# Optimization experiments

Measured on AMD Instinct MI355X. Metric: run time of the kernel, lower is better.

The kernel has to match this reference:

```python
import jax, jax.numpy as jnp
import numpy as np

BN_EPS = 1e-5
NN_EPS = 1e-8
K = 3


def conv_bn_relu(x, W, b, gamma, beta, mean, var):
    # x: [B, Cin, N]; W: [Cout, Cin] (1x1 conv); BN in inference mode w/ running stats
    y = jnp.einsum('bcn,oc->bon', x, W) + b[None, :, None]
    y = (y - mean[None, :, None]) * (gamma / jnp.sqrt(var + BN_EPS))[None, :, None] + beta[None, :, None]
    return jax.nn.relu(y)


def three_interpolation(p1, p2, f2):
    # p1: [B, N1, 3] unknown xyz; p2: [B, N2, 3] known xyz; f2: [B, C, N2]
    # squared pairwise distances via the expansion trick (avoids [B,N1,N2,3])
    d2 = (jnp.sum(p1 * p1, -1)[:, :, None]
          + jnp.sum(p2 * p2, -1)[:, None, :]
          - 2.0 * jnp.einsum('bnd,bmd->bnm', p1, p2))  # [B, N1, N2]
    neg_d2, idx = jax.lax.top_k(-d2, K)                 # 3 nearest
    dist = -neg_d2                                      # squared dists, [B, N1, 3]
    recip = 1.0 / (dist + NN_EPS)
    weight = recip / jnp.sum(recip, axis=-1, keepdims=True)  # [B, N1, 3]
    f2t = jnp.transpose(f2, (0, 2, 1))                  # [B, N2, C]
    gathered = jax.vmap(lambda f, i: f[i])(f2t, idx)    # [B, N1, 3, C]
    return jnp.einsum('bnkc,bnk->bcn', gathered, weight)  # [B, C, N1]


def setup_inputs() -> dict:
    key = jax.random.key(0)
    ks = jax.random.split(key, 16)
    B, N1, N2 = 8, 16384, 4096
    mlp = [256, 128, 128]
    inp = {
        'p1': jax.random.normal(ks[0], (B, N1, 3), jnp.float32),
        'p2': jax.random.normal(ks[1], (B, N2, 3), jnp.float32),
        'f2': jax.random.normal(ks[2], (B, mlp[0], N2), jnp.float32),
    }
    kidx = 3
    for li in range(len(mlp) - 1):
        cin, cout = mlp[li], mlp[li + 1]
        inp[f'W{li}'] = jax.random.normal(ks[kidx], (cout, cin), jnp.float32) * (1.0 / np.sqrt(cin)); kidx += 1
        inp[f'b{li}'] = jnp.zeros((cout,), jnp.float32)
        inp[f'gamma{li}'] = jnp.ones((cout,), jnp.float32)
        inp[f'beta{li}'] = jnp.zeros((cout,), jnp.float32)
        inp[f'mean{li}'] = jax.random.normal(ks[kidx], (cout,), jnp.float32) * 0.1; kidx += 1
        inp[f'var{li}'] = jax.random.uniform(ks[kidx], (cout,), jnp.float32, 0.5, 1.5); kidx += 1
    return inp


def reference(p1, p2, f2,
              W0, b0, gamma0, beta0, mean0, var0,
              W1, b1, gamma1, beta1, mean1, var1):
    f = conv_bn_relu(f2, W0, b0, gamma0, beta0, mean0, var0)
    f = conv_bn_relu(f, W1, b1, gamma1, beta1, mean1, var1)
    return three_interpolation(p1, p2, f)
```

## Files before the change

kernel.cpp:

```cpp
#include <hip/hip_runtime.h>

#define B_    8
#define N1_   16384
#define N2_   4096
#define NTOT_ (B_ * N1_)

__device__ __forceinline__ float np_sumsq(float x, float y, float z)
{
#pragma clang fp contract(off)
    return ((x * x + y * y) + z * z);
}

__global__ __launch_bounds__(256) void fold_kernel(
    const float* __restrict__ W, const float* __restrict__ bias,
    const float* __restrict__ gamma, const float* __restrict__ beta,
    const float* __restrict__ mean, const float* __restrict__ var,
    float* __restrict__ Wp, float* __restrict__ bp, int Cout, int Cin)
{
    int t = blockIdx.x * 256 + threadIdx.x;
    if (t < Cout * Cin) {
        int o = t / Cin;
        float s = gamma[o] / sqrtf(var[o] + 1e-5f);
        Wp[t] = W[t] * s;
    }
    if (t < Cout) {
        float s = gamma[t] / sqrtf(var[t] + 1e-5f);
        bp[t] = beta[t] + (bias[t] - mean[t]) * s;
    }
}

__global__ __launch_bounds__(256) void q4_kernel(
    const float* __restrict__ p2, float4* __restrict__ q4)
{
    int t = blockIdx.x * 256 + threadIdx.x;
    float x = p2[3 * (size_t)t + 0];
    float y = p2[3 * (size_t)t + 1];
    float z = p2[3 * (size_t)t + 2];
    q4[t] = make_float4(x, y, z, np_sumsq(x, y, z));
}

template <int CIN, bool TRANS>
__global__ __launch_bounds__(256) void gemm_relu_kernel(
    const float* __restrict__ X, const float* __restrict__ Wp,
    const float* __restrict__ bp, float* __restrict__ Y)
{
    __shared__ float A_lds[32][136];
    __shared__ float B_lds[32][128];

    const int b  = blockIdx.y;
    const int n0 = blockIdx.x * 128;
    const int tid = threadIdx.x;
    const int ty = tid >> 4;
    const int tx = tid & 15;
    const float* Xb = X + (size_t)b * CIN * N2_;

    float acc[8][8];
#pragma unroll
    for (int i = 0; i < 8; ++i)
#pragma unroll
        for (int j = 0; j < 8; ++j) acc[i][j] = 0.f;

    const int a_kq = (tid & 7) * 4;
    const int a_r0 = tid >> 3;
    const int b_n4 = (tid & 31) * 4;
    const int b_k0 = tid >> 5;

    for (int k0 = 0; k0 < CIN; k0 += 32) {
#pragma unroll
        for (int i = 0; i < 4; ++i) {
            const int row = a_r0 + 32 * i;
            const float4 v = *(const float4*)&Wp[(size_t)row * CIN + k0 + a_kq];
            A_lds[a_kq + 0][row] = v.x;
            A_lds[a_kq + 1][row] = v.y;
            A_lds[a_kq + 2][row] = v.z;
            A_lds[a_kq + 3][row] = v.w;
        }
#pragma unroll
        for (int i = 0; i < 4; ++i) {
            const int krow = b_k0 + 8 * i;
            *(float4*)&B_lds[krow][b_n4] =
                *(const float4*)&Xb[(size_t)(k0 + krow) * N2_ + n0 + b_n4];
        }
        __syncthreads();

#pragma unroll
        for (int kk = 0; kk < 32; ++kk) {
            const float4 a0 = *(const float4*)&A_lds[kk][ty * 4];
            const float4 a1 = *(const float4*)&A_lds[kk][64 + ty * 4];
            const float4 bq0 = *(const float4*)&B_lds[kk][tx * 4];
            const float4 bq1 = *(const float4*)&B_lds[kk][64 + tx * 4];
            const float av[8] = {a0.x, a0.y, a0.z, a0.w, a1.x, a1.y, a1.z, a1.w};
            const float bv[8] = {bq0.x, bq0.y, bq0.z, bq0.w, bq1.x, bq1.y, bq1.z, bq1.w};
#pragma unroll
            for (int i = 0; i < 8; ++i)
#pragma unroll
                for (int j = 0; j < 8; ++j)
                    acc[i][j] = fmaf(av[i], bv[j], acc[i][j]);
        }
        __syncthreads();
    }

    float bias_v[8];
#pragma unroll
    for (int i = 0; i < 8; ++i) {
        const int r = (i < 4) ? (ty * 4 + i) : (64 + ty * 4 + (i - 4));
        bias_v[i] = bp[r];
    }

    if (!TRANS) {
#pragma unroll
        for (int i = 0; i < 8; ++i) {
            const int r = (i < 4) ? (ty * 4 + i) : (64 + ty * 4 + (i - 4));
            float* yrow = Y + ((size_t)b * 128 + r) * N2_ + n0;
            float4 v0, v1;
            v0.x = fmaxf(acc[i][0] + bias_v[i], 0.f);
            v0.y = fmaxf(acc[i][1] + bias_v[i], 0.f);
            v0.z = fmaxf(acc[i][2] + bias_v[i], 0.f);
            v0.w = fmaxf(acc[i][3] + bias_v[i], 0.f);
            v1.x = fmaxf(acc[i][4] + bias_v[i], 0.f);
            v1.y = fmaxf(acc[i][5] + bias_v[i], 0.f);
            v1.z = fmaxf(acc[i][6] + bias_v[i], 0.f);
            v1.w = fmaxf(acc[i][7] + bias_v[i], 0.f);
            *(float4*)(yrow + tx * 4) = v0;
            *(float4*)(yrow + 64 + tx * 4) = v1;
        }
    } else {
        float (*T)[132] = (float(*)[132])&A_lds[0][0];
#pragma unroll
        for (int s = 0; s < 4; ++s) {
            if ((tx >> 3) == (s & 1)) {
                const int joff = (s >> 1) * 4;
                const int cl0 = (tx & 7) * 4;
#pragma unroll
                for (int i = 0; i < 8; ++i) {
                    const int r = (i < 4) ? (ty * 4 + i) : (64 + ty * 4 + (i - 4));
#pragma unroll
                    for (int j = 0; j < 4; ++j)
                        T[cl0 + j][r] = fmaxf(acc[i][j + joff] + bias_v[i], 0.f);
                }
            }
            __syncthreads();
#pragma unroll
            for (int p = 0; p < 4; ++p) {
                const int row = (tid >> 5) + 8 * p;
                const float4 v = *(const float4*)&T[row][(tid & 31) * 4];
                float* orow = Y + ((size_t)b * N2_ + n0 + 32 * s + row) * 128;
                *(float4*)&orow[(tid & 31) * 4] = v;
            }
            __syncthreads();
        }
    }
}

__global__ __launch_bounds__(256, 8) void knn_phase1(
    const float* __restrict__ p1, const float4* __restrict__ q4,
    float* __restrict__ part_d, int* __restrict__ part_i)
{
    __shared__ float4 qs[1024];
    const int tid = threadIdx.x;
    const int chunk = blockIdx.x & 3;
    const int g = (blockIdx.x >> 2) * 256 + tid;
    const int b = g >> 14;

    const float px = p1[3 * (size_t)g + 0];
    const float py = p1[3 * (size_t)g + 1];
    const float pz = p1[3 * (size_t)g + 2];
    const float s1 = np_sumsq(px, py, pz);

    const float4* qb = q4 + (size_t)b * N2_ + chunk * 1024;
#pragma unroll
    for (int i = 0; i < 4; ++i) qs[tid + i * 256] = qb[tid + i * 256];
    __syncthreads();

    float d0 = 1e30f, d1 = 1e30f, d2v = 1e30f;
    int i0 = 0, i1 = 0, i2 = 0;
    const int jbase = chunk * 1024;

    for (int j = 0; j < 1024; j += 4) {
#pragma unroll
        for (int u = 0; u < 4; ++u) {
            const float4 q = qs[j + u];
            const float dot = __fmaf_rn(px, q.x, __fmaf_rn(py, q.y, __fmul_rn(pz, q.z)));
            const float ss  = s1 + q.w;
            const float t   = __fmaf_rn(-2.0f, dot, ss);
            if (t < d2v) {
                const int jj = jbase + j + u;
                const bool c1 = t < d1, c0 = t < d0;
                d2v = c1 ? d1 : t;                 i2 = c1 ? i1 : jj;
                const float nd1 = c1 ? (c0 ? d0 : t) : d1;
                const int   ni1 = c1 ? (c0 ? i0 : jj) : i1;
                d1 = nd1;                          i1 = ni1;
                d0 = c0 ? t : d0;                  i0 = c0 ? jj : i0;
            }
        }
    }

    part_d[(0 * 4 + chunk) * NTOT_ + g] = d0;
    part_d[(1 * 4 + chunk) * NTOT_ + g] = d1;
    part_d[(2 * 4 + chunk) * NTOT_ + g] = d2v;
    part_i[(0 * 4 + chunk) * NTOT_ + g] = i0;
    part_i[(1 * 4 + chunk) * NTOT_ + g] = i1;
    part_i[(2 * 4 + chunk) * NTOT_ + g] = i2;
}

__global__ __launch_bounds__(256) void knn_merge(
    const float* __restrict__ part_d, const int* __restrict__ part_i,
    int* __restrict__ idx_ws, float* __restrict__ w_ws)
{
    const int g = blockIdx.x * 256 + threadIdx.x;

    float d0 = 1e30f, d1 = 1e30f, d2v = 1e30f;
    int i0 = 0, i1 = 0, i2 = 0;

#pragma unroll
    for (int c = 0; c < 4; ++c) {
#pragma unroll
        for (int k = 0; k < 3; ++k) {
            const float t = part_d[(k * 4 + c) * NTOT_ + g];
            const int  jj = part_i[(k * 4 + c) * NTOT_ + g];
            if (t < d2v) {
                const bool c1 = t < d1, c0 = t < d0;
                d2v = c1 ? d1 : t;                 i2 = c1 ? i1 : jj;
                const float nd1 = c1 ? (c0 ? d0 : t) : d1;
                const int   ni1 = c1 ? (c0 ? i0 : jj) : i1;
                d1 = nd1;                          i1 = ni1;
                d0 = c0 ? t : d0;                  i0 = c0 ? jj : i0;
            }
        }
    }

    float w0, w1, w2;
    {
#pragma clang fp contract(off)
        const float r0 = 1.0f / (d0 + 1e-8f);
        const float r1 = 1.0f / (d1 + 1e-8f);
        const float r2 = 1.0f / (d2v + 1e-8f);
        const float rs = (r0 + r1) + r2;
        w0 = r0 / rs;
        w1 = r1 / rs;
        w2 = r2 / rs;
    }

    idx_ws[g]             = i0;
    idx_ws[NTOT_ + g]     = i1;
    idx_ws[2 * NTOT_ + g] = i2;
    w_ws[g]               = w0;
    w_ws[NTOT_ + g]       = w1;
    w_ws[2 * NTOT_ + g]   = w2;
}

__global__ __launch_bounds__(256) void gather_kernel(
    const float* __restrict__ f_t, const int* __restrict__ idx_ws,
    const float* __restrict__ w_ws, float* __restrict__ out)
{
    const int tid = threadIdx.x;
    const int lane = tid & 63, cg = tid >> 6;
    const int g = blockIdx.x * 64 + lane;
    const int b = g >> 14, n = g & 16383;

    const int i0 = idx_ws[g];
    const int i1 = idx_ws[NTOT_ + g];
    const int i2 = idx_ws[2 * NTOT_ + g];
    const float w0 = w_ws[g];
    const float w1 = w_ws[NTOT_ + g];
    const float w2 = w_ws[2 * NTOT_ + g];

    const float* base = f_t + (size_t)b * N2_ * 128 + cg * 32;
    const float4* r0 = (const float4*)(base + (size_t)i0 * 128);
    const float4* r1 = (const float4*)(base + (size_t)i1 * 128);
    const float4* r2 = (const float4*)(base + (size_t)i2 * 128);

    float acc[32];
#pragma unroll
    for (int q = 0; q < 8; ++q) {
        const float4 a = r0[q], bb = r1[q], c = r2[q];
        acc[4 * q + 0] = fmaf(w0, a.x, fmaf(w1, bb.x, w2 * c.x));
        acc[4 * q + 1] = fmaf(w0, a.y, fmaf(w1, bb.y, w2 * c.y));
        acc[4 * q + 2] = fmaf(w0, a.z, fmaf(w1, bb.z, w2 * c.z));
        acc[4 * q + 3] = fmaf(w0, a.w, fmaf(w1, bb.w, w2 * c.w));
    }

    float* ob = out + ((size_t)b * 128 + cg * 32) * N1_ + n;
#pragma unroll
    for (int c = 0; c < 32; ++c)
        __builtin_nontemporal_store(acc[c], ob + (size_t)c * N1_);
}

extern "C" void kernel_launch(void* const* d_in, const int* in_sizes, int n_in,
                              void* d_out, int out_size, void* d_ws, size_t ws_size,
                              hipStream_t stream)
{
    const float* p1  = (const float*)d_in[0];
    const float* p2  = (const float*)d_in[1];
    const float* f2  = (const float*)d_in[2];
    const float* W0  = (const float*)d_in[3];
    const float* b0  = (const float*)d_in[4];
    const float* g0  = (const float*)d_in[5];
    const float* be0 = (const float*)d_in[6];
    const float* m0  = (const float*)d_in[7];
    const float* v0  = (const float*)d_in[8];
    const float* W1  = (const float*)d_in[9];
    const float* b1  = (const float*)d_in[10];
    const float* g1  = (const float*)d_in[11];
    const float* be1 = (const float*)d_in[12];
    const float* m1  = (const float*)d_in[13];
    const float* v1  = (const float*)d_in[14];

    char* ws = (char*)d_ws;
    float4* q4  = (float4*)(ws);
    float*  W0p = (float*)(ws + (512 << 10));
    float*  b0p = (float*)(ws + (640 << 10));
    float*  W1p = (float*)(ws + (644 << 10));
    float*  b1p = (float*)(ws + (708 << 10));
    float*  h   = (float*)(ws + ((size_t)1 << 20));
    float*  f_t = (float*)(ws + ((size_t)17 << 20));
    int*    idxw= (int*)  (ws + ((size_t)33 << 20));
    float*  wgt = (float*)(ws + ((size_t)35 << 20));
    float*  pd  = (float*)(ws + ((size_t)1 << 20));
    int*    pi  = (int*)  (ws + ((size_t)9 << 20));

    fold_kernel<<<128, 256, 0, stream>>>(W0, b0, g0, be0, m0, v0, W0p, b0p, 128, 256);
    fold_kernel<<<64, 256, 0, stream>>>(W1, b1, g1, be1, m1, v1, W1p, b1p, 128, 128);
    q4_kernel<<<(B_ * N2_) / 256, 256, 0, stream>>>(p2, q4);

    gemm_relu_kernel<256, false><<<dim3(32, 8), 256, 0, stream>>>(f2, W0p, b0p, h);
    gemm_relu_kernel<128, true ><<<dim3(32, 8), 256, 0, stream>>>(h, W1p, b1p, f_t);

    knn_phase1<<<(NTOT_ / 256) * 4, 256, 0, stream>>>(p1, q4, pd, pi);
    knn_merge<<<NTOT_ / 256, 256, 0, stream>>>(pd, pi, idxw, wgt);
    gather_kernel<<<NTOT_ / 64, 256, 0, stream>>>(f_t, idxw, wgt, (float*)d_out);
}
```

Baseline: 354.5 us.

## Fuse KNN split-merge into one kernel with packed-FP32 distance pairs

Replaces the 4-way chunked KNN pass and its separate merge kernel with a single kernel. Each thread now scans all 4096 reference points, streamed into LDS in four chunks. Reference points are repacked in pairs (x0,x1,y0,y1,z0,z1,w0,w1) so that distances are computed with 2-wide vector FMAs, which can map to packed FP32 ops. The top-3 insertion is skipped when no lane in the wavefront has a candidate. This removes the partial-result round trip to global memory and one launch. In exchange there are 4x fewer blocks, so each thread does a longer serial loop, and the launch-bounds occupancy hint is dropped.

```diff
diff --git a/kernel.cpp b/kernel.cpp
--- a/kernel.cpp
+++ b/kernel.cpp
@@ -4,6 +4,8 @@
 #define N1_   16384
 #define N2_   4096
 #define NTOT_ (B_ * N1_)
+
+typedef float v2f __attribute__((ext_vector_type(2)));
 
 __device__ __forceinline__ float np_sumsq(float x, float y, float z)
 {
@@ -29,14 +31,16 @@
     }
 }
 
-__global__ __launch_bounds__(256) void q4_kernel(
-    const float* __restrict__ p2, float4* __restrict__ q4)
-{
-    int t = blockIdx.x * 256 + threadIdx.x;
-    float x = p2[3 * (size_t)t + 0];
-    float y = p2[3 * (size_t)t + 1];
-    float z = p2[3 * (size_t)t + 2];
-    q4[t] = make_float4(x, y, z, np_sumsq(x, y, z));
+__global__ __launch_bounds__(256) void q4pair_kernel(
+    const float* __restrict__ p2, float4* __restrict__ q4p)
+{
+    const int t = blockIdx.x * 256 + threadIdx.x;
+    const float* a = p2 + 6 * (size_t)t;
+    const float x0 = a[0], y0 = a[1], z0 = a[2];
+    const float x1 = a[3], y1 = a[4], z1 = a[5];
+    q4p[2 * (size_t)t + 0] = make_float4(x0, x1, y0, y1);
+    q4p[2 * (size_t)t + 1] = make_float4(z0, z1, np_sumsq(x0, y0, z0),
+                                                 np_sumsq(x1, y1, z1));
 }
 
 template <int CIN, bool TRANS>
@@ -152,14 +156,28 @@
     }
 }
 
-__global__ __launch_bounds__(256, 8) void knn_phase1(
-    const float* __restrict__ p1, const float4* __restrict__ q4,
-    float* __restrict__ part_d, int* __restrict__ part_i)
-{
-    __shared__ float4 qs[1024];
+__device__ __forceinline__ void ins3(const float t, const int jj,
+    float& d0, float& d1, float& d2v, int& i0, int& i1, int& i2)
+{
+    if (t < d2v) {
+        const bool c1 = t < d1, c0 = t < d0;
+        d2v = c1 ? d1 : t;                 i2 = c1 ? i1 : jj;
+        const float nd1 = c1 ? (c0 ? d0 : t) : d1;
+        const int   ni1 = c1 ? (c0 ? i0 : jj) : i1;
+        d1 = nd1;                          i1 = ni1;
+        d0 = c0 ? t : d0;                  i0 = c0 ? jj : i0;
+    }
+}
+
+__global__ __launch_bounds__(256) void knn_fused(
+    const float* __restrict__ p1, const float4* __restrict__ q4p,
+    int* __restrict__ idx_ws, float* __restrict__ w_ws)
+{
+#pragma clang fp contract(off)
+    __shared__ float4 qpk[512][2];
+
     const int tid = threadIdx.x;
-    const int chunk = blockIdx.x & 3;
-    const int g = (blockIdx.x >> 2) * 256 + tid;
+    const int g = blockIdx.x * 256 + tid;
     const int b = g >> 14;
 
     const float px = p1[3 * (size_t)g + 0];
@@ -167,79 +185,63 @@
     const float pz = p1[3 * (size_t)g + 2];
     const float s1 = np_sumsq(px, py, pz);
 
-    const float4* qb = q4 + (size_t)b * N2_ + chunk * 1024;
-#pragma unroll
-    for (int i = 0; i < 4; ++i) qs[tid + i * 256] = qb[tid + i * 256];
-    __syncthreads();
+    const v2f px2 = {px, px};
+    const v2f py2 = {py, py};
+    const v2f pz2 = {pz, pz};
+    const v2f s12 = {s1, s1};
+    const v2f m2  = {-2.0f, -2.0f};
 
     float d0 = 1e30f, d1 = 1e30f, d2v = 1e30f;
     int i0 = 0, i1 = 0, i2 = 0;
-    const int jbase = chunk * 1024;
-
-    for (int j = 0; j < 1024; j += 4) {
-#pragma unroll
-        for (int u = 0; u < 4; ++u) {
-            const float4 q = qs[j + u];
-            const float dot = __fmaf_rn(px, q.x, __fmaf_rn(py, q.y, __fmul_rn(pz, q.z)));
-            const float ss  = s1 + q.w;
-            const float t   = __fmaf_rn(-2.0f, dot, ss);
-            if (t < d2v) {
-                const int jj = jbase + j + u;
-                const bool c1 = t < d1, c0 = t < d0;
-                d2v = c1 ? d1 : t;                 i2 = c1 ? i1 : jj;
-                const float nd1 = c1 ? (c0 ? d0 : t) : d1;
-                const int   ni1 = c1 ? (c0 ? i0 : jj) : i1;
-                d1 = nd1;                          i1 = ni1;
-                d0 = c0 ? t : d0;                  i0 = c0 ? jj : i0;
+
+    const float4* qb = q4p + (size_t)b * N2_;
+
+    for (int c = 0; c < 4; ++c) {
+        if (c) __syncthreads();
+#pragma unroll
+        for (int i = 0; i < 2; ++i) {
+            const int p = tid + i * 256;
+            qpk[p][0] = qb[(size_t)(c * 512 + p) * 2 + 0];
+            qpk[p][1] = qb[(size_t)(c * 512 + p) * 2 + 1];
+        }
+        __syncthreads();
+
+        const int jb = c * 1024;
+        for (int p4 = 0; p4 < 512; p4 += 4) {
+            v2f tt[4];
+#pragma unroll
+            for (int u = 0; u < 4; ++u) {
+                const float4 A  = qpk[p4 + u][0];
+                const float4 Bq = qpk[p4 + u][1];
+                const v2f x01 = {A.x, A.y};
+                const v2f y01 = {A.z, A.w};
+                const v2f z01 = {Bq.x, Bq.y};
+                const v2f w01 = {Bq.z, Bq.w};
+                const v2f zz  = z01 * pz2;
+                const v2f dot = __builtin_elementwise_fma(px2, x01,
+                                  __builtin_elementwise_fma(py2, y01, zz));
+                const v2f ss  = s12 + w01;
+                tt[u] = __builtin_elementwise_fma(m2, dot, ss);
             }
-        }
-    }
-
-    part_d[(0 * 4 + chunk) * NTOT_ + g] = d0;
-    part_d[(1 * 4 + chunk) * NTOT_ + g] = d1;
-    part_d[(2 * 4 + chunk) * NTOT_ + g] = d2v;
-    part_i[(0 * 4 + chunk) * NTOT_ + g] = i0;
-    part_i[(1 * 4 + chunk) * NTOT_ + g] = i1;
-    part_i[(2 * 4 + chunk) * NTOT_ + g] = i2;
-}
-
-__global__ __launch_bounds__(256) void knn_merge(
-    const float* __restrict__ part_d, const int* __restrict__ part_i,
-    int* __restrict__ idx_ws, float* __restrict__ w_ws)
-{
-    const int g = blockIdx.x * 256 + threadIdx.x;
-
-    float d0 = 1e30f, d1 = 1e30f, d2v = 1e30f;
-    int i0 = 0, i1 = 0, i2 = 0;
-
-#pragma unroll
-    for (int c = 0; c < 4; ++c) {
-#pragma unroll
-        for (int k = 0; k < 3; ++k) {
-            const float t = part_d[(k * 4 + c) * NTOT_ + g];
-            const int  jj = part_i[(k * 4 + c) * NTOT_ + g];
-            if (t < d2v) {
-                const bool c1 = t < d1, c0 = t < d0;
-                d2v = c1 ? d1 : t;                 i2 = c1 ? i1 : jj;
-                const float nd1 = c1 ? (c0 ? d0 : t) : d1;
-                const int   ni1 = c1 ? (c0 ? i0 : jj) : i1;
-                d1 = nd1;                          i1 = ni1;
-                d0 = c0 ? t : d0;                  i0 = c0 ? jj : i0;
+#pragma unroll
+            for (int u = 0; u < 4; ++u) {
+                const float t0 = tt[u].x, t1 = tt[u].y;
+                if (__any(fminf(t0, t1) < d2v)) {
+                    const int j0 = jb + 2 * (p4 + u);
+                    ins3(t0, j0,     d0, d1, d2v, i0, i1, i2);
+                    ins3(t1, j0 + 1, d0, d1, d2v, i0, i1, i2);
+                }
             }
         }
     }
 
-    float w0, w1, w2;
-    {
-#pragma clang fp contract(off)
-        const float r0 = 1.0f / (d0 + 1e-8f);
-        const float r1 = 1.0f / (d1 + 1e-8f);
-        const float r2 = 1.0f / (d2v + 1e-8f);
-        const float rs = (r0 + r1) + r2;
-        w0 = r0 / rs;
-        w1 = r1 / rs;
-        w2 = r2 / rs;
-    }
+    const float r0 = 1.0f / (d0 + 1e-8f);
+    const float r1 = 1.0f / (d1 + 1e-8f);
+    const float r2 = 1.0f / (d2v + 1e-8f);
+    const float rs = (r0 + r1) + r2;
+    const float w0 = r0 / rs;
+    const float w1 = r1 / rs;
+    const float w2 = r2 / rs;
 
     idx_ws[g]             = i0;
     idx_ws[NTOT_ + g]     = i1;
@@ -307,7 +309,7 @@
     const float* v1  = (const float*)d_in[14];
 
     char* ws = (char*)d_ws;
-    float4* q4  = (float4*)(ws);
+    float4* q4p = (float4*)(ws);
     float*  W0p = (float*)(ws + (512 << 10));
     float*  b0p = (float*)(ws + (640 << 10));
     float*  W1p = (float*)(ws + (644 << 10));
@@ -316,17 +318,14 @@
     float*  f_t = (float*)(ws + ((size_t)17 << 20));
     int*    idxw= (int*)  (ws + ((size_t)33 << 20));
     float*  wgt = (float*)(ws + ((size_t)35 << 20));
-    float*  pd  = (float*)(ws + ((size_t)1 << 20));
-    int*    pi  = (int*)  (ws + ((size_t)9 << 20));
 
     fold_kernel<<<128, 256, 0, stream>>>(W0, b0, g0, be0, m0, v0, W0p, b0p, 128, 256);
     fold_kernel<<<64, 256, 0, stream>>>(W1, b1, g1, be1, m1, v1, W1p, b1p, 128, 128);
-    q4_kernel<<<(B_ * N2_) / 256, 256, 0, stream>>>(p2, q4);
+    q4pair_kernel<<<(B_ * N2_ / 2) / 256, 256, 0, stream>>>(p2, q4p);
 
     gemm_relu_kernel<256, false><<<dim3(32, 8), 256, 0, stream>>>(f2, W0p, b0p, h);
     gemm_relu_kernel<128, true ><<<dim3(32, 8), 256, 0, stream>>>(h, W1p, b1p, f_t);
 
-    knn_phase1<<<(NTOT_ / 256) * 4, 256, 0, stream>>>(p1, q4, pd, pi);
-    knn_merge<<<NTOT_ / 256, 256, 0, stream>>>(pd, pi, idxw, wgt);
+    knn_fused<<<NTOT_ / 256, 256, 0, stream>>>(p1, q4p, idxw, wgt);
     gather_kernel<<<NTOT_ / 64, 256, 0, stream>>>(f_t, idxw, wgt, (float*)d_out);
 }
```

Result: slower. 379.3 us (+7.0%).

## Pack reference points in pairs for packed-FP32 distance math in KNN

Applied to the files above, without the earlier changes.

Reference points are repacked into two planar float4 arrays holding pairs of points, so the KNN distance loop can evaluate two candidates per packed-float2 FMA (v_pk_fma_f32 on CDNA). The top-3 insertion is gated by a wave-wide __any check on the pair minimum, which moves the branch decision to wave level. The aim is to halve the ALU issue count of the distance computation in the dominant kernel. The risk is that the wave-level gate makes lanes take the insertion path more often, and that fp contract changes could shift rounding relative to the scalar version.

```diff
diff --git a/kernel.cpp b/kernel.cpp
--- a/kernel.cpp
+++ b/kernel.cpp
@@ -4,6 +4,8 @@
 #define N1_   16384
 #define N2_   4096
 #define NTOT_ (B_ * N1_)
+
+typedef float v2f __attribute__((ext_vector_type(2)));
 
 __device__ __forceinline__ float np_sumsq(float x, float y, float z)
 {
@@ -29,14 +31,16 @@
     }
 }
 
-__global__ __launch_bounds__(256) void q4_kernel(
-    const float* __restrict__ p2, float4* __restrict__ q4)
-{
-    int t = blockIdx.x * 256 + threadIdx.x;
-    float x = p2[3 * (size_t)t + 0];
-    float y = p2[3 * (size_t)t + 1];
-    float z = p2[3 * (size_t)t + 2];
-    q4[t] = make_float4(x, y, z, np_sumsq(x, y, z));
+__global__ __launch_bounds__(256) void q4planar_kernel(
+    const float* __restrict__ p2, float4* __restrict__ qA,
+    float4* __restrict__ qB)
+{
+    const int t = blockIdx.x * 256 + threadIdx.x;
+    const float* a = p2 + 6 * (size_t)t;
+    const float x0 = a[0], y0 = a[1], z0 = a[2];
+    const float x1 = a[3], y1 = a[4], z1 = a[5];
+    qA[t] = make_float4(x0, x1, y0, y1);
+    qB[t] = make_float4(z0, z1, np_sumsq(x0, y0, z0), np_sumsq(x1, y1, z1));
 }
 
 template <int CIN, bool TRANS>
@@ -152,11 +156,28 @@
     }
 }
 
+__device__ __forceinline__ void ins3(const float t, const int jj,
+    float& d0, float& d1, float& d2v, int& i0, int& i1, int& i2)
+{
+    if (t < d2v) {
+        const bool c1 = t < d1, c0 = t < d0;
+        d2v = c1 ? d1 : t;                 i2 = c1 ? i1 : jj;
+        const float nd1 = c1 ? (c0 ? d0 : t) : d1;
+        const int   ni1 = c1 ? (c0 ? i0 : jj) : i1;
+        d1 = nd1;                          i1 = ni1;
+        d0 = c0 ? t : d0;                  i0 = c0 ? jj : i0;
+    }
+}
+
 __global__ __launch_bounds__(256, 8) void knn_phase1(
-    const float* __restrict__ p1, const float4* __restrict__ q4,
+    const float* __restrict__ p1, const float4* __restrict__ qA,
+    const float4* __restrict__ qB,
     float* __restrict__ part_d, int* __restrict__ part_i)
 {
-    __shared__ float4 qs[1024];
+#pragma clang fp contract(off)
+    __shared__ float4 sA[512];
+    __shared__ float4 sB[512];
+
     const int tid = threadIdx.x;
     const int chunk = blockIdx.x & 3;
     const int g = (blockIdx.x >> 2) * 256 + tid;
@@ -167,30 +188,45 @@
     const float pz = p1[3 * (size_t)g + 2];
     const float s1 = np_sumsq(px, py, pz);
 
-    const float4* qb = q4 + (size_t)b * N2_ + chunk * 1024;
-#pragma unroll
-    for (int i = 0; i < 4; ++i) qs[tid + i * 256] = qb[tid + i * 256];
+    const v2f px2 = {px, px};
+    const v2f py2 = {py, py};
+    const v2f pz2 = {pz, pz};
+    const v2f s12 = {s1, s1};
+    const v2f m2  = {-2.0f, -2.0f};
+
+    const float4* gA = qA + (size_t)b * (N2_ / 2) + chunk * 512;
+    const float4* gB = qB + (size_t)b * (N2_ / 2) + chunk * 512;
+    sA[tid] = gA[tid];  sA[tid + 256] = gA[tid + 256];
+    sB[tid] = gB[tid];  sB[tid + 256] = gB[tid + 256];
     __syncthreads();
 
     float d0 = 1e30f, d1 = 1e30f, d2v = 1e30f;
     int i0 = 0, i1 = 0, i2 = 0;
     const int jbase = chunk * 1024;
 
-    for (int j = 0; j < 1024; j += 4) {
+    for (int p4 = 0; p4 < 512; p4 += 4) {
+        v2f tt[4];
 #pragma unroll
         for (int u = 0; u < 4; ++u) {
-            const float4 q = qs[j + u];
-            const float dot = __fmaf_rn(px, q.x, __fmaf_rn(py, q.y, __fmul_rn(pz, q.z)));
-            const float ss  = s1 + q.w;
-            const float t   = __fmaf_rn(-2.0f, dot, ss);
-            if (t < d2v) {
-                const int jj = jbase + j + u;
-                const bool c1 = t < d1, c0 = t < d0;
-                d2v = c1 ? d1 : t;                 i2 = c1 ? i1 : jj;
-                const float nd1 = c1 ? (c0 ? d0 : t) : d1;
-                const int   ni1 = c1 ? (c0 ? i0 : jj) : i1;
-                d1 = nd1;                          i1 = ni1;
-                d0 = c0 ? t : d0;                  i0 = c0 ? jj : i0;
+            const float4 A  = sA[p4 + u];
+            const float4 Bq = sB[p4 + u];
+            const v2f x01 = {A.x, A.y};
+            const v2f y01 = {A.z, A.w};
+            const v2f z01 = {Bq.x, Bq.y};
+            const v2f w01 = {Bq.z, Bq.w};
+            const v2f zz  = z01 * pz2;
+            const v2f dot = __builtin_elementwise_fma(px2, x01,
+                              __builtin_elementwise_fma(py2, y01, zz));
+            const v2f ss  = s12 + w01;
+            tt[u] = __builtin_elementwise_fma(m2, dot, ss);
+        }
+#pragma unroll
+        for (int u = 0; u < 4; ++u) {
+            const float t0 = tt[u].x, t1 = tt[u].y;
+            if (__any(fminf(t0, t1) < d2v)) {
+                const int j0 = jbase + 2 * (p4 + u);
+                ins3(t0, j0,     d0, d1, d2v, i0, i1, i2);
+                ins3(t1, j0 + 1, d0, d1, d2v, i0, i1, i2);
             }
         }
     }
@@ -307,7 +343,8 @@
     const float* v1  = (const float*)d_in[14];
 
     char* ws = (char*)d_ws;
-    float4* q4  = (float4*)(ws);
+    float4* qA  = (float4*)(ws);
+    float4* qB  = (float4*)(ws + (256 << 10));
     float*  W0p = (float*)(ws + (512 << 10));
     float*  b0p = (float*)(ws + (640 << 10));
     float*  W1p = (float*)(ws + (644 << 10));
@@ -321,12 +358,12 @@
 
     fold_kernel<<<128, 256, 0, stream>>>(W0, b0, g0, be0, m0, v0, W0p, b0p, 128, 256);
     fold_kernel<<<64, 256, 0, stream>>>(W1, b1, g1, be1, m1, v1, W1p, b1p, 128, 128);
-    q4_kernel<<<(B_ * N2_) / 256, 256, 0, stream>>>(p2, q4);
+    q4planar_kernel<<<(B_ * N2_ / 2) / 256, 256, 0, stream>>>(p2, qA, qB);
 
     gemm_relu_kernel<256, false><<<dim3(32, 8), 256, 0, stream>>>(f2, W0p, b0p, h);
     gemm_relu_kernel<128, true ><<<dim3(32, 8), 256, 0, stream>>>(h, W1p, b1p, f_t);
 
-    knn_phase1<<<(NTOT_ / 256) * 4, 256, 0, stream>>>(p1, q4, pd, pi);
+    knn_phase1<<<(NTOT_ / 256) * 4, 256, 0, stream>>>(p1, qA, qB, pd, pi);
     knn_merge<<<NTOT_ / 256, 256, 0, stream>>>(pd, pi, idxw, wgt);
     gather_kernel<<<NTOT_ / 64, 256, 0, stream>>>(f_t, idxw, wgt, (float*)d_out);
 }
```

New measurement: 358.6 us. No clear change (+1.2%).
